# Kernel optimization log

Hardware: AMD Instinct MI355X
Metric: run time of the kernel (lower is better)

The kernel has to match this reference:

```python
import jax, jax.numpy as jnp
import numpy as np

CELL_SIDE = 1.0
GRID_N = 6  # n x n occupancy grid


def _occupancy_grid(obs2):
    """Vectorized pairwise occupancy binning.
    obs2: [N, 2] -> grid [N, GRID_N*GRID_N] (counts of other pedestrians per cell)."""
    N = obs2.shape[0]
    nn = GRID_N * GRID_N
    # rel[i, j] = position of pedestrian j relative to i, in grid coords
    rel = (obs2[None, :, :] - obs2[:, None, :]) / CELL_SIDE + GRID_N / 2  # [N, N, 2]
    in_range = jnp.all((rel >= 0) & (rel < GRID_N), axis=-1)              # [N, N]
    not_self = ~jnp.eye(N, dtype=bool)
    valid = ~jnp.isnan(obs2[:, 0])                                        # [N]
    mask = in_range & not_self & valid[:, None] & valid[None, :]
    ij = jnp.clip(rel.astype(jnp.int32), 0, GRID_N - 1)                   # floor (rel>=0 under mask)
    local_bin = ij[..., 0] * GRID_N + ij[..., 1]                          # [N, N]
    # Global segment id: row i owns bins [i*nn, (i+1)*nn); invalid -> trash bin N*nn
    seg = jnp.where(mask, jnp.arange(N, dtype=jnp.int32)[:, None] * nn + local_bin, N * nn)
    counts = jax.ops.segment_sum(mask.astype(jnp.float32).reshape(-1),
                                 seg.reshape(-1), num_segments=N * nn + 1)
    return counts[: N * nn].reshape(N, nn)


def setup_inputs() -> dict:
    key = jax.random.key(0)
    k1, k2, k3, k4, k5 = jax.random.split(key, 5)
    N, hidden_dim, nn = 8192, 128, GRID_N * GRID_N
    hidden_state = jax.random.normal(k1, (N, hidden_dim), dtype=jnp.float32)
    obs1 = jax.random.normal(k2, (N, 2), dtype=jnp.float32)
    obs2 = jax.random.normal(k3, (N, 2), dtype=jnp.float32)
    W = jax.random.normal(k4, (hidden_dim, nn), dtype=jnp.float32) * (1.0 / np.sqrt(nn))
    b = jax.random.normal(k5, (hidden_dim,), dtype=jnp.float32) * 0.01
    return {"hidden_state": hidden_state, "obs1": obs1, "obs2": obs2, "W": W, "b": b}


def reference(hidden_state, obs1, obs2, W, b):
    # type_='occupancy': grid depends only on obs2; then Linear embedding.
    grid = _occupancy_grid(obs2)              # [N, 36]
    return grid @ W.T + b                     # [N, 128]
```

## Files before the change

kernel.cpp:

```cpp
#include <hip/hip_runtime.h>

#define N_PED  8192
#define HID    128
#define NN     36
#define IPB    8
#define SLICES 64
#define BLOCK  512
#define JS     128
#define HWW    9
#define NB     1024

__global__ __launch_bounds__(BLOCK, 8) void pool_kernel(
    const float* __restrict__ obs2_g,
    const float* __restrict__ Wg,
    const float* __restrict__ bias,
    float* __restrict__ out)
{
    __shared__ unsigned s_hA[HWW * BLOCK];
    __shared__ unsigned s_hB[HWW * BLOCK];
    __shared__ float    s_rgrid[IPB][NN];
    __shared__ unsigned s_wsel[IPB];

    const int tid = threadIdx.x;
    const int bid = blockIdx.x;

    #pragma unroll
    for (int k = 0; k < HWW; ++k) {
        s_hA[tid + k * BLOCK] = 0u;
        s_hB[tid + k * BLOCK] = 0u;
    }

    const int il    = tid & (IPB - 1);
    const int slice = tid >> 3;
    const int i     = bid * IPB + il;

    const float2 pi = ((const float2*)obs2_g)[i];
    const float  xi4 = pi.x - 4.0f;
    const float  yi4 = pi.y - 4.0f;

    if (tid < IPB) {
        float dx = pi.x - xi4;
        float dy = pi.y - yi4;
        unsigned u1 = (unsigned)((int)dx) - 1u;
        unsigned u2 = (unsigned)((int)dy) - 1u;
        bool ok = (u1 < 6u) & (u2 < 6u);
        s_wsel[il] = ok ? (u1 * 6u + u2) : 255u;
    }
    __syncthreads();

    #define PAIR(H, px, py) do {                                    \
        float dx = (px) - xi4;                                      \
        float dy = (py) - yi4;                                      \
        unsigned u1 = (unsigned)((int)dx) - 1u;                     \
        unsigned u2 = (unsigned)((int)dy) - 1u;                     \
        unsigned mx = u1 > u2 ? u1 : u2;                            \
        bool ok = mx < 6u;                                          \
        unsigned bin = (u1 << 2) + ((u1 << 1) + u2);                \
        unsigned w   = ok ? (bin >> 2) : 0u;                        \
        unsigned inc = ok ? (1u << ((bin << 3) & 24u)) : 0u;        \
        H[(w << 9) + tid] += inc;                                   \
    } while (0)

    #define PAIR8(r0, r1, r2, r3) do {                              \
        PAIR(s_hA, r0.x, r0.y); PAIR(s_hB, r0.z, r0.w);             \
        PAIR(s_hA, r1.x, r1.y); PAIR(s_hB, r1.z, r1.w);             \
        PAIR(s_hA, r2.x, r2.y); PAIR(s_hB, r2.z, r2.w);             \
        PAIR(s_hA, r3.x, r3.y); PAIR(s_hB, r3.z, r3.w);             \
    } while (0)

    {
        const float4* jp = (const float4*)obs2_g + slice * (JS / 2);
        float4 a0 = jp[0], a1 = jp[1], a2 = jp[2], a3 = jp[3];
        float4 b0 = jp[4], b1 = jp[5], b2 = jp[6], b3 = jp[7];
        jp += 8;
        #pragma unroll 1
        for (int it = 0; it < 7; ++it) {
            PAIR8(a0, a1, a2, a3);
            a0 = jp[0]; a1 = jp[1]; a2 = jp[2]; a3 = jp[3];
            PAIR8(b0, b1, b2, b3);
            b0 = jp[4]; b1 = jp[5]; b2 = jp[6]; b3 = jp[7];
            jp += 8;
        }
        PAIR8(a0, a1, a2, a3);
        PAIR8(b0, b1, b2, b3);
    }
    #undef PAIR8
    #undef PAIR
    __syncthreads();

    if (tid < IPB * HWW) {
        const int ril = tid & (IPB - 1);
        const int w   = tid >> 3;
        unsigned lo = 0u, hi = 0u;
        #pragma unroll 8
        for (int sl = 0; sl < SLICES; ++sl) {
            unsigned t = sl * IPB + ril;
            unsigned a = s_hA[(w << 9) + t];
            unsigned b = s_hB[(w << 9) + t];
            lo += (a & 0x00FF00FFu) + (b & 0x00FF00FFu);
            hi += ((a >> 8) & 0x00FF00FFu) + ((b >> 8) & 0x00FF00FFu);
        }
        unsigned s0 = lo & 0xFFFFu;
        unsigned s1 = hi & 0xFFFFu;
        unsigned s2 = lo >> 16;
        unsigned s3 = hi >> 16;
        const unsigned sel  = s_wsel[ril];
        const unsigned base = (unsigned)(w * 4);
        s0 -= (sel == base + 0u);
        s1 -= (sel == base + 1u);
        s2 -= (sel == base + 2u);
        s3 -= (sel == base + 3u);
        s_rgrid[ril][base + 0] = (float)s0;
        s_rgrid[ril][base + 1] = (float)s1;
        s_rgrid[ril][base + 2] = (float)s2;
        s_rgrid[ril][base + 3] = (float)s3;
    }
    __syncthreads();

    const int h  = tid & (HID - 1);
    const int r0 = tid >> 7;
    const float4* W4 = (const float4*)Wg;

    const float bh = bias[h];
    float acc0 = bh, acc1 = bh;

    #pragma unroll
    for (int k4 = 0; k4 < 9; ++k4) {
        float4 w4 = W4[h * 9 + k4];
        float4 g0 = *(const float4*)&s_rgrid[r0    ][k4 * 4];
        float4 g1 = *(const float4*)&s_rgrid[r0 + 4][k4 * 4];
        acc0 += g0.x * w4.x + g0.y * w4.y + g0.z * w4.z + g0.w * w4.w;
        acc1 += g1.x * w4.x + g1.y * w4.y + g1.z * w4.z + g1.w * w4.w;
    }

    const int obase = bid * IPB;
    out[(obase + r0    ) * HID + h] = acc0;
    out[(obase + r0 + 4) * HID + h] = acc1;
}

extern "C" void kernel_launch(void* const* d_in, const int* in_sizes, int n_in,
                              void* d_out, int out_size, void* d_ws, size_t ws_size,
                              hipStream_t stream) {
    const float* obs2 = (const float*)d_in[2];
    const float* W    = (const float*)d_in[3];
    const float* b    = (const float*)d_in[4];
    float* out        = (float*)d_out;
    (void)in_sizes; (void)n_in; (void)out_size; (void)d_ws; (void)ws_size;

    hipLaunchKernelGGL(pool_kernel, dim3(NB), dim3(BLOCK), 0, stream,
                       obs2, W, b, out);
}
```

Baseline: 41.89 us.

## Replace LDS histogram increments with register bit-sliced carry-save counters

Each pair is now turned into a 64-bit one-hot bin mask, and the masks are summed into seven bit-plane registers with carry-save adders. The per-pair read-modify-write on shared memory and the histogram zeroing are gone. The bit planes are converted once per thread into packed byte counts in a single shared histogram, which the existing reduction then sums. In exchange there is more ALU work on 64-bit values and higher register pressure, and launch bounds drop from 8 to 4 blocks per SM.

```diff
diff --git a/kernel.cpp b/kernel.cpp
--- a/kernel.cpp
+++ b/kernel.cpp
@@ -7,28 +7,55 @@
 #define SLICES 64
 #define BLOCK  512
 #define JS     128
-#define HWW    9
 #define NB     1024
 
-__global__ __launch_bounds__(BLOCK, 8) void pool_kernel(
+typedef unsigned long long u64;
+typedef unsigned u32;
+
+#define CSA(s, r, a, b, c) do { u64 _a=(a), _b=(b), _c=(c); u64 _t=_a^_b; \
+    (r) = (_a & _b) | (_t & _c); (s) = _t ^ _c; } while (0)
+
+__device__ __forceinline__ u64 onehot(float px, float py, float xi4, float yi4) {
+    float dx = px - xi4;
+    float dy = py - yi4;
+    u32 u1 = (u32)((int)dx) - 1u;
+    u32 u2 = (u32)((int)dy) - 1u;
+    u32 mx = u1 > u2 ? u1 : u2;
+    u32 bin = u1 * 6u + u2;
+    bin = (mx < 6u) ? bin : 63u;
+    return 1ull << bin;
+}
+
+__device__ __forceinline__ void add8(
+    u64 x0, u64 x1, u64 x2, u64 x3, u64 x4, u64 x5, u64 x6, u64 x7,
+    u64& R1, u64& R2, u64& R4, u64& R8, u64& R16, u64& R32, u64& R64)
+{
+    u64 s0,c0,s1,c1,s2,c2,c3,s4,c4,c5,c6,c7,c8,c9;
+    CSA(s0, c0, x0, x1, x2);
+    CSA(s1, c1, x3, x4, x5);
+    CSA(s2, c2, x6, x7, s0);
+    CSA(R1, c3, s1, s2, R1);
+    CSA(s4, c4, c0, c1, c2);
+    CSA(R2, c5, s4, c3, R2);
+    CSA(R4, c6, c4, c5, R4);
+    c7 = R8  & c6;  R8  ^= c6;
+    c8 = R16 & c7;  R16 ^= c7;
+    c9 = R32 & c8;  R32 ^= c8;
+    R64 |= c9;
+}
+
+__global__ __launch_bounds__(BLOCK, 4) void pool_kernel(
     const float* __restrict__ obs2_g,
     const float* __restrict__ Wg,
     const float* __restrict__ bias,
     float* __restrict__ out)
 {
-    __shared__ unsigned s_hA[HWW * BLOCK];
-    __shared__ unsigned s_hB[HWW * BLOCK];
-    __shared__ float    s_rgrid[IPB][NN];
-    __shared__ unsigned s_wsel[IPB];
+    __shared__ u32  s_h[9 * BLOCK];
+    __shared__ float s_rgrid[IPB][NN];
+    __shared__ u32  s_wsel[IPB];
 
     const int tid = threadIdx.x;
     const int bid = blockIdx.x;
-
-    #pragma unroll
-    for (int k = 0; k < HWW; ++k) {
-        s_hA[tid + k * BLOCK] = 0u;
-        s_hB[tid + k * BLOCK] = 0u;
-    }
 
     const int il    = tid & (IPB - 1);
     const int slice = tid >> 3;
@@ -41,32 +68,20 @@
     if (tid < IPB) {
         float dx = pi.x - xi4;
         float dy = pi.y - yi4;
-        unsigned u1 = (unsigned)((int)dx) - 1u;
-        unsigned u2 = (unsigned)((int)dy) - 1u;
+        u32 u1 = (u32)((int)dx) - 1u;
+        u32 u2 = (u32)((int)dy) - 1u;
         bool ok = (u1 < 6u) & (u2 < 6u);
         s_wsel[il] = ok ? (u1 * 6u + u2) : 255u;
     }
-    __syncthreads();
 
-    #define PAIR(H, px, py) do {                                    \
-        float dx = (px) - xi4;                                      \
-        float dy = (py) - yi4;                                      \
-        unsigned u1 = (unsigned)((int)dx) - 1u;                     \
-        unsigned u2 = (unsigned)((int)dy) - 1u;                     \
-        unsigned mx = u1 > u2 ? u1 : u2;                            \
-        bool ok = mx < 6u;                                          \
-        unsigned bin = (u1 << 2) + ((u1 << 1) + u2);                \
-        unsigned w   = ok ? (bin >> 2) : 0u;                        \
-        unsigned inc = ok ? (1u << ((bin << 3) & 24u)) : 0u;        \
-        H[(w << 9) + tid] += inc;                                   \
-    } while (0)
+    u64 R1=0, R2=0, R4=0, R8=0, R16=0, R32=0, R64=0;
 
-    #define PAIR8(r0, r1, r2, r3) do {                              \
-        PAIR(s_hA, r0.x, r0.y); PAIR(s_hB, r0.z, r0.w);             \
-        PAIR(s_hA, r1.x, r1.y); PAIR(s_hB, r1.z, r1.w);             \
-        PAIR(s_hA, r2.x, r2.y); PAIR(s_hB, r2.z, r2.w);             \
-        PAIR(s_hA, r3.x, r3.y); PAIR(s_hB, r3.z, r3.w);             \
-    } while (0)
+    #define GRP8(r0, r1, r2, r3)                                         \
+        add8(onehot(r0.x, r0.y, xi4, yi4), onehot(r0.z, r0.w, xi4, yi4), \
+             onehot(r1.x, r1.y, xi4, yi4), onehot(r1.z, r1.w, xi4, yi4), \
+             onehot(r2.x, r2.y, xi4, yi4), onehot(r2.z, r2.w, xi4, yi4), \
+             onehot(r3.x, r3.y, xi4, yi4), onehot(r3.z, r3.w, xi4, yi4), \
+             R1, R2, R4, R8, R16, R32, R64)
 
     {
         const float4* jp = (const float4*)obs2_g + slice * (JS / 2);
@@ -75,37 +90,53 @@
         jp += 8;
         #pragma unroll 1
         for (int it = 0; it < 7; ++it) {
-            PAIR8(a0, a1, a2, a3);
+            GRP8(a0, a1, a2, a3);
             a0 = jp[0]; a1 = jp[1]; a2 = jp[2]; a3 = jp[3];
-            PAIR8(b0, b1, b2, b3);
+            GRP8(b0, b1, b2, b3);
             b0 = jp[4]; b1 = jp[5]; b2 = jp[6]; b3 = jp[7];
             jp += 8;
         }
-        PAIR8(a0, a1, a2, a3);
-        PAIR8(b0, b1, b2, b3);
+        GRP8(a0, a1, a2, a3);
+        GRP8(b0, b1, b2, b3);
     }
-    #undef PAIR8
-    #undef PAIR
+    #undef GRP8
+
+    {
+        const u32 lo[7] = { (u32)R1,  (u32)R2,  (u32)R4,  (u32)R8,
+                            (u32)R16, (u32)R32, (u32)R64 };
+        const u32 hi[7] = { (u32)(R1>>32),  (u32)(R2>>32),  (u32)(R4>>32),
+                            (u32)(R8>>32),  (u32)(R16>>32), (u32)(R32>>32),
+                            (u32)(R64>>32) };
+        #pragma unroll
+        for (int w = 0; w < 9; ++w) {
+            u32 acc = 0;
+            #pragma unroll
+            for (int L = 0; L < 7; ++L) {
+                u32 nib = (w < 8) ? ((lo[L] >> (4 * w)) & 0xFu)
+                                  : (hi[L] & 0xFu);
+                acc += ((nib * 0x00204081u) & 0x01010101u) << L;
+            }
+            s_h[w * BLOCK + tid] = acc;
+        }
+    }
     __syncthreads();
 
-    if (tid < IPB * HWW) {
+    if (tid < IPB * 9) {
         const int ril = tid & (IPB - 1);
         const int w   = tid >> 3;
-        unsigned lo = 0u, hi = 0u;
+        u32 lo = 0u, hi = 0u;
         #pragma unroll 8
         for (int sl = 0; sl < SLICES; ++sl) {
-            unsigned t = sl * IPB + ril;
-            unsigned a = s_hA[(w << 9) + t];
-            unsigned b = s_hB[(w << 9) + t];
-            lo += (a & 0x00FF00FFu) + (b & 0x00FF00FFu);
-            hi += ((a >> 8) & 0x00FF00FFu) + ((b >> 8) & 0x00FF00FFu);
+            u32 a = s_h[(w << 9) + sl * IPB + ril];
+            lo += a & 0x00FF00FFu;
+            hi += (a >> 8) & 0x00FF00FFu;
         }
-        unsigned s0 = lo & 0xFFFFu;
-        unsigned s1 = hi & 0xFFFFu;
-        unsigned s2 = lo >> 16;
-        unsigned s3 = hi >> 16;
-        const unsigned sel  = s_wsel[ril];
-        const unsigned base = (unsigned)(w * 4);
+        u32 s0 = lo & 0xFFFFu;
+        u32 s1 = hi & 0xFFFFu;
+        u32 s2 = lo >> 16;
+        u32 s3 = hi >> 16;
+        const u32 sel  = s_wsel[ril];
+        const u32 base = (u32)(w * 4);
         s0 -= (sel == base + 0u);
         s1 -= (sel == base + 1u);
         s2 -= (sel == base + 2u);
```

After: 50.05 us. +19.5%, slower.
